# Optimization experiments

Hardware: AMD Instinct MI355X
Metric: run time of the kernel (lower is better)

The kernel has to match this reference:

```python
import jax, jax.numpy as jnp
import numpy as np

DIM = 50
K = 51  # kernel_size == DIM + 1 (required by the original view())
E = 6   # num_elems
NT = 29 # num_targets
B = 8
DN = ('NCDHW', 'OIDHW', 'NCDHW')


def setup_inputs() -> dict:
    key = jax.random.key(0)
    ks = jax.random.split(key, 14)
    f = jnp.float32
    inp = {
        'x': jax.random.uniform(ks[0], (B, E, DIM, DIM, DIM), dtype=f),
        'sigma': 3.0 * jnp.ones((E,), dtype=f),
        'w1': jax.random.normal(ks[1], (32, E, 3, 3, 3), dtype=f) * 0.1,
        'b1': jnp.full((32,), 0.01, dtype=f),
        'w2': jax.random.normal(ks[2], (64, 32, 3, 3, 3), dtype=f) * 0.05,
        'b2': jnp.full((64,), 0.01, dtype=f),
        'w3': jax.random.normal(ks[3], (128, 64, 3, 3, 3), dtype=f) * 0.05,
        'b3': jnp.full((128,), 0.01, dtype=f),
        'w4': jax.random.normal(ks[4], (256, 128, 3, 3, 3), dtype=f) * 0.03,
        'b4': jnp.full((256,), 0.01, dtype=f),
        'fw1': jax.random.normal(ks[5], (128, 256), dtype=f) * 0.06,
        'fb1': jnp.full((128,), 0.01, dtype=f),
        'fw2': jax.random.normal(ks[6], (NT, 128), dtype=f) * 0.08,
        'fb2': jnp.full((NT,), 0.01, dtype=f),
    }
    return inp


def _blur_kernel(sigma):
    # Gauss transformation kernel, shape (E, 1, K, K, K)
    c = jnp.arange(K, dtype=jnp.float32)
    mean = (K - 1) / 2.0
    d2 = (c - mean) ** 2
    # squared radius grid (K,K,K), symmetric so the torch transpose(3,0) axis swap is a no-op
    r2 = d2[:, None, None] + d2[None, :, None] + d2[None, None, :]
    var = sigma ** 2  # (E,)
    a = 1.0 / (2.0 * np.pi * var)  # (E,)
    kern = a[:, None, None, None] * jnp.exp(-r2[None] / (2.0 * var)[:, None, None, None])
    kern = kern / jnp.sum(kern)  # normalize by GLOBAL sum (as in torch code)
    return kern[:, None]  # (E,1,K,K,K)


def _conv3(x, w, b):
    y = jax.lax.conv_general_dilated(x, w, (1, 1, 1), 'VALID', dimension_numbers=DN)
    return y + b[None, :, None, None, None]


def _pool(x):
    return jax.lax.reduce_window(x, -jnp.inf, jax.lax.max,
                                 (1, 1, 2, 2, 2), (1, 1, 2, 2, 2), 'VALID')


def reference(x, sigma, w1, b1, w2, b2, w3, b3, w4, b4, fw1, fb1, fw2, fb2):
    # blur: grouped 3D conv with on-the-fly Gaussian kernel, padding 25 keeps DIM
    kern = _blur_kernel(sigma)
    pad = (K - 1) // 2
    xc = jax.lax.conv_general_dilated(x, kern, (1, 1, 1), [(pad, pad)] * 3,
                                      feature_group_count=E, dimension_numbers=DN)
    xc = xc / jnp.max(xc)
    # conv stack: (conv -> pool -> relu) x4
    h = jax.nn.relu(_pool(_conv3(xc, w1, b1)))   # (B,32,24,24,24)
    h = jax.nn.relu(_pool(_conv3(h, w2, b2)))    # (B,64,11,11,11)
    h = jax.nn.relu(_pool(_conv3(h, w3, b3)))    # (B,128,4,4,4)
    h = jax.nn.relu(_pool(_conv3(h, w4, b4)))    # (B,256,1,1,1)
    v = h.reshape(x.shape[0], -1)                # (B,256)
    y1 = jax.nn.relu(v @ fw1.T + fb1)
    return y1 @ fw2.T + fb2                      # (B,29)
```

## Files before the change

### kernel.cpp

```cpp
#include <hip/hip_runtime.h>
#include <math.h>

#define DIMX 50
#define KK   51
#define NE   6
#define NB   8
#define NVOX ((size_t)NB * NE * DIMX * DIMX * DIMX)

typedef short bf16x8 __attribute__((ext_vector_type(8)));
typedef float f32x4  __attribute__((ext_vector_type(4)));

__device__ __forceinline__ unsigned short f2bf(float f) {
    unsigned u = __float_as_uint(f);
    u += 0x7fffu + ((u >> 16) & 1u);
    return (unsigned short)(u >> 16);
}
__device__ __forceinline__ float bf2f(unsigned short h) {
    return __uint_as_float((unsigned)h << 16);
}
__device__ __forceinline__ uint4 pack8(const unsigned short v[8]) {
    uint4 q;
    q.x = v[0] | ((unsigned)v[1] << 16);
    q.y = v[2] | ((unsigned)v[3] << 16);
    q.z = v[4] | ((unsigned)v[5] << 16);
    q.w = v[6] | ((unsigned)v[7] << 16);
    return q;
}
__device__ __forceinline__ int offA(int o, int k) {
    return ((((o >> 4) * 2 + (k >> 5)) * 64 + ((k >> 3) & 3) * 16 + (o & 15)) << 3) + (k & 7);
}

__global__ void taps_kernel(const float* __restrict__ sigma,
                            unsigned short* __restrict__ MA, unsigned short* __restrict__ MB,
                            float* __restrict__ maxval) {
    __shared__ float sg[NE * KK];
    __shared__ float sgs[NE * KK];
    __shared__ float ssum[NE];
    int t = threadIdx.x;
    if (t == 0) *maxval = 0.f;
    if (t < NE * KK) {
        int e = t / KK, i = t % KK;
        float d = (float)i - 25.0f;
        float var = sigma[e] * sigma[e];
        sg[t] = expf(-d * d / (2.f * var));
    }
    __syncthreads();
    if (t < NE) {
        float s = 0.f;
        for (int i = 0; i < KK; ++i) s += sg[t * KK + i];
        ssum[t] = s;
    }
    __syncthreads();
    if (t < NE * KK) {
        int e = t / KK;
        float S = 0.f;
        for (int e2 = 0; e2 < NE; ++e2) {
            float var2 = sigma[e2] * sigma[e2];
            float a2 = 1.f / (2.f * (float)M_PI * var2);
            float se = ssum[e2];
            S += a2 * se * se * se;
        }
        float var = sigma[e] * sigma[e];
        float a = 1.f / (2.f * (float)M_PI * var);
        sgs[t] = sg[t] * (a / S);
    }
    __syncthreads();
    const int TOT = 2 * 6 * 4 * 2 * 64 * 8;
    for (int i = t; i < 2 * TOT; i += 512) {
        int which = i / TOT;
        int r = i % TOT;
        int q = r;
        int j = q & 7; q >>= 3;
        int l = q & 63; q >>= 6;
        int kc = q & 1; q >>= 1;
        int tile = q & 3; q >>= 2;
        int e = q % 6; q /= 6;
        int hl = q;
        int own = tile * 16 + (l & 15);
        int k   = kc * 32 + ((l >> 4) << 3) + j;
        float v = 0.f;
        if (own < 50 && k < 50) {
            int d = k - own + 25;
            if (d >= 0 && d < KK) v = (which == 0 ? sg : sgs)[e * KK + d];
        }
        unsigned short h = f2bf(v);
        unsigned short out = (hl == 0) ? h : f2bf(v - bf2f(h));
        (which == 0 ? MA : MB)[r] = out;
    }
}

__global__ __launch_bounds__(64)
void blur_k1(const float* __restrict__ in, float* __restrict__ W1,
             const unsigned short* __restrict__ MA) {
    const int l = threadIdx.x, lm = l & 15, lg = l >> 4;
    const int y = blockIdx.x % 50, be = blockIdx.x / 50, e = be % 6;
    const float* pb = in + (size_t)be * 125000 + y * 50;
    bf16x8 Ah[4][2], Al[4][2];
#pragma unroll
    for (int ozt = 0; ozt < 4; ++ozt)
#pragma unroll
        for (int kc = 0; kc < 2; ++kc) {
            Ah[ozt][kc] = *(const bf16x8*)(MA + (((size_t)(0 * 6 + e) * 4 + ozt) * 2 + kc) * 512 + l * 8);
            Al[ozt][kc] = *(const bf16x8*)(MA + (((size_t)(1 * 6 + e) * 4 + ozt) * 2 + kc) * 512 + l * 8);
        }
    float* ob = W1 + (size_t)be * 125000 + y * 50;
    const f32x4 z4 = {0.f, 0.f, 0.f, 0.f};
#pragma unroll 1
    for (int xt = 0; xt < 4; ++xt) {
        const int xx = xt * 16 + lm;
        bf16x8 bh[2], bl[2];
#pragma unroll
        for (int kc = 0; kc < 2; ++kc) {
            unsigned short vh[8], vl[8];
#pragma unroll
            for (int j = 0; j < 8; ++j) {
                int z = kc * 32 + lg * 8 + j;
                float v = (z < 50 && xx < 50) ? pb[(size_t)z * 2500 + xx] : 0.f;
                unsigned short h = f2bf(v);
                vh[j] = h; vl[j] = f2bf(v - bf2f(h));
            }
            uint4 qh = pack8(vh), ql = pack8(vl);
            bh[kc] = *(bf16x8*)&qh; bl[kc] = *(bf16x8*)&ql;
        }
        f32x4 acc[4];
#pragma unroll
        for (int ozt = 0; ozt < 4; ++ozt) acc[ozt] = z4;
#pragma unroll
        for (int ozt = 0; ozt < 4; ++ozt)
#pragma unroll
            for (int kc = 0; kc < 2; ++kc) {
                acc[ozt] = __builtin_amdgcn_mfma_f32_16x16x32_bf16(Ah[ozt][kc], bh[kc], acc[ozt], 0, 0, 0);
                acc[ozt] = __builtin_amdgcn_mfma_f32_16x16x32_bf16(Ah[ozt][kc], bl[kc], acc[ozt], 0, 0, 0);
                acc[ozt] = __builtin_amdgcn_mfma_f32_16x16x32_bf16(Al[ozt][kc], bh[kc], acc[ozt], 0, 0, 0);
            }
        if (xx < 50) {
#pragma unroll
            for (int ozt = 0; ozt < 4; ++ozt)
#pragma unroll
                for (int i = 0; i < 4; ++i) {
                    int oz = ozt * 16 + lg * 4 + i;
                    if (oz < 50) ob[(size_t)oz * 2500 + xx] = acc[ozt][i];
                }
        }
    }
}

__global__ __launch_bounds__(64)
void blur_k2(const float* __restrict__ W1, const unsigned short* __restrict__ MA,
             const unsigned short* __restrict__ MB, unsigned short* __restrict__ X1,
             float* __restrict__ maxval) {
    __shared__ unsigned short Qhi[4096], Qlo[4096];
    const int l = threadIdx.x, lm = l & 15, lg = l >> 4;
    const int q8 = (int)(gridDim.x >> 3);
    const int logical = ((int)blockIdx.x & 7) * q8 + ((int)blockIdx.x >> 3);
    const int e = logical % 6, bz = logical / 6, z = bz % 50, b = bz / 50;
    const float* pb = W1 + (size_t)(b * 6 + e) * 125000 + (size_t)z * 2500;
    bf16x8 Bh[4][2], Bl[4][2];
#pragma unroll
    for (int xt = 0; xt < 4; ++xt) {
        const int xx = xt * 16 + lm;
#pragma unroll
        for (int kc = 0; kc < 2; ++kc) {
            unsigned short vh[8], vl[8];
#pragma unroll
            for (int j = 0; j < 8; ++j) {
                int yy = kc * 32 + lg * 8 + j;
                float v = (yy < 50 && xx < 50) ? pb[yy * 50 + xx] : 0.f;
                unsigned short h = f2bf(v);
                vh[j] = h; vl[j] = f2bf(v - bf2f(h));
            }
            uint4 qh = pack8(vh), ql = pack8(vl);
            Bh[xt][kc] = *(bf16x8*)&qh; Bl[xt][kc] = *(bf16x8*)&ql;
        }
    }
    const f32x4 z4 = {0.f, 0.f, 0.f, 0.f};
#pragma unroll 1
    for (int oyt = 0; oyt < 4; ++oyt) {
        bf16x8 Ah[2], Al[2];
#pragma unroll
        for (int kc = 0; kc < 2; ++kc) {
            Ah[kc] = *(const bf16x8*)(MA + (((size_t)(0 * 6 + e) * 4 + oyt) * 2 + kc) * 512 + l * 8);
            Al[kc] = *(const bf16x8*)(MA + (((size_t)(1 * 6 + e) * 4 + oyt) * 2 + kc) * 512 + l * 8);
        }
#pragma unroll
        for (int xt = 0; xt < 4; ++xt) {
            f32x4 acc = z4;
#pragma unroll
            for (int kc = 0; kc < 2; ++kc) {
                acc = __builtin_amdgcn_mfma_f32_16x16x32_bf16(Ah[kc], Bh[xt][kc], acc, 0, 0, 0);
                acc = __builtin_amdgcn_mfma_f32_16x16x32_bf16(Ah[kc], Bl[xt][kc], acc, 0, 0, 0);
                acc = __builtin_amdgcn_mfma_f32_16x16x32_bf16(Al[kc], Bh[xt][kc], acc, 0, 0, 0);
            }
#pragma unroll
            for (int i = 0; i < 4; ++i) {
                int oy = oyt * 16 + lg * 4 + i;
                int xx = xt * 16 + lm;
                float qv = acc[i];
                unsigned short h = f2bf(qv);
                int off = offA(oy, xx);
                Qhi[off] = h; Qlo[off] = f2bf(qv - bf2f(h));
            }
        }
    }
    __builtin_amdgcn_wave_barrier();
    asm volatile("s_waitcnt lgkmcnt(0)" ::: "memory");
    __builtin_amdgcn_sched_barrier(0);
    float mmax = 0.f;
    unsigned short* xb = X1 + ((size_t)b * 125000 + (size_t)z * 2500) * 8 + e;
#pragma unroll 1
    for (int oyt = 0; oyt < 4; ++oyt) {
        bf16x8 Qh[2], Ql[2];
#pragma unroll
        for (int kc = 0; kc < 2; ++kc) {
            Qh[kc] = *(const bf16x8*)(Qhi + ((oyt * 2 + kc) * 64 + l) * 8);
            Ql[kc] = *(const bf16x8*)(Qlo + ((oyt * 2 + kc) * 64 + l) * 8);
        }
#pragma unroll
        for (int oxt = 0; oxt < 4; ++oxt) {
            f32x4 acc = z4;
#pragma unroll
            for (int kc = 0; kc < 2; ++kc) {
                bf16x8 mh = *(const bf16x8*)(MB + (((size_t)(0 * 6 + e) * 4 + oxt) * 2 + kc) * 512 + l * 8);
                bf16x8 ml = *(const bf16x8*)(MB + (((size_t)(1 * 6 + e) * 4 + oxt) * 2 + kc) * 512 + l * 8);
                acc = __builtin_amdgcn_mfma_f32_16x16x32_bf16(Qh[kc], mh, acc, 0, 0, 0);
                acc = __builtin_amdgcn_mfma_f32_16x16x32_bf16(Qh[kc], ml, acc, 0, 0, 0);
                acc = __builtin_amdgcn_mfma_f32_16x16x32_bf16(Ql[kc], mh, acc, 0, 0, 0);
            }
            int ox = oxt * 16 + lm;
            if (ox < 50) {
#pragma unroll
                for (int i = 0; i < 4; ++i) {
                    int oy = oyt * 16 + lg * 4 + i;
                    if (oy < 50) {
                        float r = acc[i];
                        xb[((size_t)oy * 50 + ox) * 8] = f2bf(r);
                        mmax = fmaxf(mmax, r);
                    }
                }
            }
        }
    }
    for (int o = 32; o; o >>= 1) mmax = fmaxf(mmax, __shfl_xor(mmax, o));
    if (l == 0) atomicMax((int*)maxval, __float_as_int(mmax));
}

__global__ void wprep_kernel(const float* __restrict__ W, unsigned short* __restrict__ out,
                             int CIN, int NCH, int NCOG) {
    int idx = blockIdx.x * 256 + threadIdx.x;
    int total = NCOG * 27 * NCH * 64;
    if (idx >= total) return;
    int l = idx & 63;
    int r = idx >> 6;
    int ch = r % NCH; r /= NCH;
    int tap = r % 27;
    int cog = r / 27;
    int co = cog * 16 + (l & 15);
    unsigned short v[8];
#pragma unroll
    for (int j = 0; j < 8; ++j) {
        int ci = ch * 32 + (l >> 4) * 8 + j;
        v[j] = (ci < CIN) ? f2bf(W[((size_t)co * CIN + ci) * 27 + tap]) : (unsigned short)0;
    }
    ((uint4*)out)[idx] = pack8(v);
}

__global__ void wprep1_kernel(const float* __restrict__ W, unsigned short* __restrict__ out) {
    int idx = blockIdx.x * 64 + threadIdx.x;
    if (idx >= 2 * 9 * 64) return;
    int l = idx & 63;
    int r = idx >> 6;
    int tg = r % 9;
    int cog = r / 9;
    int xsel = l >> 4;
    int co = cog * 16 + (l & 15);
    unsigned short v[8];
#pragma unroll
    for (int j = 0; j < 8; ++j) {
        float wv = 0.f;
        if (j < 6 && xsel < 3) wv = W[((size_t)co * 6 + j) * 27 + tg * 3 + xsel];
        v[j] = f2bf(wv);
    }
    ((uint4*)out)[idx] = pack8(v);
}

__global__ __launch_bounds__(64, 3)
void conv1_mfma(const unsigned short* __restrict__ X8, const unsigned short* __restrict__ wp1,
                const float* __restrict__ bias, const float* __restrict__ maxval,
                unsigned short* __restrict__ X2) {
    const int l = threadIdx.x, lm = l & 15, lg = l >> 4;
    const int q = (int)(gridDim.x >> 3);
    const int bid = ((int)blockIdx.x & 7) * q + ((int)blockIdx.x >> 3);
    const int s0 = bid * 8;
    const int r0 = s0 / 72;
    const int cog = r0 % 2;
    const int pz  = (r0 / 2) % 24;
    const int b   = r0 / 48;
    uint4 B9[9];
    const uint4* wpb = (const uint4*)wp1 + cog * 9 * 64;
#pragma unroll
    for (int t = 0; t < 9; ++t) B9[t] = wpb[t * 64 + l];
    const float rmv = 1.0f / (*maxval);
    const float bia = bias[cog * 16 + lm];
    const unsigned short* Xb = X8 + (size_t)b * 125000 * 8;
    const f32x4 z4 = {0.f, 0.f, 0.f, 0.f};
#pragma unroll 1
    for (int si = 0; si < 8; ++si) {
        const int sid = s0 + si;
        const int xs = sid % 3;
        const int py = (sid / 3) % 24;
        const int x0 = xs * 16;
        f32x4 acc[2][2];
#pragma unroll
        for (int cz = 0; cz < 2; ++cz)
#pragma unroll
            for (int cy = 0; cy < 2; ++cy) acc[cz][cy] = z4;
#pragma unroll
        for (int zi = 0; zi < 4; ++zi) {
            const int zin = 2 * pz + zi;
#pragma unroll
            for (int yi = 0; yi < 4; ++yi) {
                const int yin = 2 * py + yi;
                const unsigned short* rowb = Xb + (size_t)(zin * 50 + yin) * 50 * 8;
                bf16x8 a = *(const bf16x8*)(rowb + (x0 + lm + lg) * 8);
#pragma unroll
                for (int cz = 0; cz < 2; ++cz) {
                    const int kz = zi - cz;
                    if (kz < 0 || kz > 2) continue;
#pragma unroll
                    for (int cy = 0; cy < 2; ++cy) {
                        const int ky = yi - cy;
                        if (ky < 0 || ky > 2) continue;
                        acc[cz][cy] = __builtin_amdgcn_mfma_f32_16x16x32_bf16(
                            a, *(const bf16x8*)&B9[kz * 3 + ky], acc[cz][cy], 0, 0, 0);
                    }
                }
            }
        }
        const int co = cog * 16 + lm;
#pragma unroll
        for (int ip = 0; ip < 2; ++ip) {
            float m0 = fmaxf(fmaxf(acc[0][0][2 * ip], acc[0][1][2 * ip]),
                             fmaxf(acc[1][0][2 * ip], acc[1][1][2 * ip]));
            float m1 = fmaxf(fmaxf(acc[0][0][2 * ip + 1], acc[0][1][2 * ip + 1]),
                             fmaxf(acc[1][0][2 * ip + 1], acc[1][1][2 * ip + 1]));
            float o = fmaxf(fmaxf(m0, m1) * rmv + bia, 0.f);
            int px = x0 / 2 + lg * 2 + ip;
            X2[((((size_t)b * 24 + pz) * 24 + py) * 24 + px) * 32 + co] = f2bf(o);
        }
    }
}

template <int DIN, int DP, int CI, int NCH, int NCOG, int NPY, int NXS, int SPB, int NPZ>
__global__ __launch_bounds__(64, 3)
void convN_mfma(const unsigned short* __restrict__ X, const unsigned short* __restrict__ wp,
                const float* __restrict__ bias, unsigned short* __restrict__ Y, int COUT) {
    const int l = threadIdx.x, lm = l & 15, lg = l >> 4;
    const int qq = (int)(gridDim.x >> 3);
    const int bid = ((int)blockIdx.x & 7) * qq + ((int)blockIdx.x >> 3);
    const int s0 = bid * SPB;
    const int r0 = s0 / (NPY * NXS);
    const int cog = r0 % NCOG;
    const int pz  = (r0 / NCOG) % NPZ;
    const int b   = r0 / (NCOG * NPZ);
    const float bia = bias[cog * 16 + lm];
    const unsigned short* Xb = X + (size_t)b * DIN * DIN * DIN * CI;
    const uint4* wp4 = (const uint4*)wp;
    const f32x4 z4 = {0.f, 0.f, 0.f, 0.f};
#pragma unroll 1
    for (int si = 0; si < SPB; ++si) {
        const int sid = s0 + si;
        const int xs = sid % NXS;
        const int py = (sid / NXS) % NPY;
        const int x0 = xs * 16;
        int xo[3];
#pragma unroll
        for (int kx = 0; kx < 3; ++kx) {
            int xin = x0 + kx + lm;
            if (xin > DIN - 1) xin = DIN - 1;
            xo[kx] = xin * CI + lg * 8;
        }
        f32x4 acc[2][2];
#pragma unroll
        for (int cz = 0; cz < 2; ++cz)
#pragma unroll
            for (int cy = 0; cy < 2; ++cy) acc[cz][cy] = z4;
#pragma unroll 1
        for (int ch = 0; ch < NCH; ++ch) {
            uint4 B[27];
            const uint4* wpb = wp4 + ((size_t)cog * 27 * NCH + ch) * 64;
#pragma unroll
            for (int t = 0; t < 27; ++t) B[t] = wpb[(size_t)t * NCH * 64 + l];
            const unsigned short* Xc = Xb + ch * 32;
#pragma unroll
            for (int zi = 0; zi < 4; ++zi) {
                const int zin = 2 * pz + zi;
#pragma unroll
                for (int yi = 0; yi < 4; ++yi) {
                    const int yin = 2 * py + yi;
                    const unsigned short* rowb = Xc + (size_t)(zin * DIN + yin) * DIN * CI;
#pragma unroll
                    for (int kx = 0; kx < 3; ++kx) {
                        bf16x8 a = *(const bf16x8*)(rowb + xo[kx]);
#pragma unroll
                        for (int cz = 0; cz < 2; ++cz) {
                            const int kz = zi - cz;
                            if (kz < 0 || kz > 2) continue;
#pragma unroll
                            for (int cy = 0; cy < 2; ++cy) {
                                const int ky = yi - cy;
                                if (ky < 0 || ky > 2) continue;
                                const int tap = (kz * 3 + ky) * 3 + kx;
                                acc[cz][cy] = __builtin_amdgcn_mfma_f32_16x16x32_bf16(
                                    a, *(const bf16x8*)&B[tap], acc[cz][cy], 0, 0, 0);
                            }
                        }
                    }
                }
            }
        }
        const int co = cog * 16 + lm;
#pragma unroll
        for (int ip = 0; ip < 2; ++ip) {
            float m0 = fmaxf(fmaxf(acc[0][0][2 * ip], acc[0][1][2 * ip]),
                             fmaxf(acc[1][0][2 * ip], acc[1][1][2 * ip]));
            float m1 = fmaxf(fmaxf(acc[0][0][2 * ip + 1], acc[0][1][2 * ip + 1]),
                             fmaxf(acc[1][0][2 * ip + 1], acc[1][1][2 * ip + 1]));
            float o = fmaxf(fmaxf(m0, m1) + bia, 0.f);
            int px = x0 / 2 + lg * 2 + ip;
            if (px < DP)
                Y[((((size_t)b * DP + pz) * DP + py) * DP + px) * COUT + co] = f2bf(o);
        }
    }
}

__global__ void conv4_kernel(const unsigned short* __restrict__ X4, const float* __restrict__ w,
                             const float* __restrict__ bias, float* __restrict__ out) {
    int wid = (int)((blockIdx.x * blockDim.x + threadIdx.x) >> 6);
    int lane = threadIdx.x & 63;
    if (wid >= NB * 256) return;
    int b = wid >> 8, co = wid & 255;
    float acc[8];
#pragma unroll
    for (int i = 0; i < 8; ++i) acc[i] = 0.f;
    for (int half = 0; half < 2; ++half) {
        int ci = lane + half * 64;
        float win[64];
#pragma unroll
        for (int v = 0; v < 64; ++v)
            win[v] = bf2f(X4[((size_t)b * 64 + v) * 128 + ci]);
        const float* wc = w + ((size_t)co * 128 + ci) * 27;
        float wr[27];
#pragma unroll
        for (int i = 0; i < 27; ++i) wr[i] = wc[i];
#pragma unroll
        for (int kz = 0; kz < 3; ++kz)
#pragma unroll
            for (int ky = 0; ky < 3; ++ky)
#pragma unroll
                for (int kx = 0; kx < 3; ++kx) {
                    float wv = wr[(kz * 3 + ky) * 3 + kx];
#pragma unroll
                    for (int oz = 0; oz < 2; ++oz)
#pragma unroll
                        for (int oy = 0; oy < 2; ++oy)
#pragma unroll
                            for (int ox = 0; ox < 2; ++ox)
                                acc[(oz * 2 + oy) * 2 + ox] =
                                    fmaf(wv, win[((oz + kz) * 4 + (oy + ky)) * 4 + ox + kx],
                                         acc[(oz * 2 + oy) * 2 + ox]);
                }
    }
#pragma unroll
    for (int o = 32; o; o >>= 1)
#pragma unroll
        for (int i = 0; i < 8; ++i) acc[i] += __shfl_xor(acc[i], o);
    if (lane == 0) {
        float m = acc[0];
#pragma unroll
        for (int i = 1; i < 8; ++i) m = fmaxf(m, acc[i]);
        out[(size_t)b * 256 + co] = fmaxf(m + bias[co], 0.f);
    }
}

__global__ void head_kernel(const float* __restrict__ v,
                            const float* __restrict__ fw1, const float* __restrict__ fb1,
                            const float* __restrict__ fw2, const float* __restrict__ fb2,
                            float* __restrict__ out) {
    int b = blockIdx.x, t = threadIdx.x;
    __shared__ float sv[256];
    __shared__ float s1[128];
    sv[t] = v[b * 256 + t];
    sv[t + 128] = v[b * 256 + t + 128];
    __syncthreads();
    float acc = fb1[t];
    const float* wr = fw1 + t * 256;
    for (int k = 0; k < 256; ++k) acc = fmaf(wr[k], sv[k], acc);
    s1[t] = fmaxf(acc, 0.f);
    __syncthreads();
    if (t < 29) {
        float a2 = fb2[t];
        const float* w2 = fw2 + t * 128;
        for (int k = 0; k < 128; ++k) a2 = fmaf(w2[k], s1[k], a2);
        out[b * 29 + t] = a2;
    }
}

extern "C" void kernel_launch(void* const* d_in, const int* in_sizes, int n_in,
                              void* d_out, int out_size, void* d_ws, size_t ws_size,
                              hipStream_t stream) {
    const float* x     = (const float*)d_in[0];
    const float* sigma = (const float*)d_in[1];
    const float* w1    = (const float*)d_in[2];
    const float* b1    = (const float*)d_in[3];
    const float* w2    = (const float*)d_in[4];
    const float* b2    = (const float*)d_in[5];
    const float* w3    = (const float*)d_in[6];
    const float* b3    = (const float*)d_in[7];
    const float* w4    = (const float*)d_in[8];
    const float* b4    = (const float*)d_in[9];
    const float* fw1   = (const float*)d_in[10];
    const float* fb1   = (const float*)d_in[11];
    const float* fw2   = (const float*)d_in[12];
    const float* fb2   = (const float*)d_in[13];
    float* out = (float*)d_out;

    float* W1 = (float*)d_ws;
    unsigned short* X1  = (unsigned short*)(W1 + NVOX);
    unsigned short* X2  = X1 + 8000064;
    unsigned short* X3  = X2 + 3538944;
    unsigned short* X4  = X3 + 681472;
    unsigned short* wp1 = X4 + 65536;
    unsigned short* wp2 = wp1 + 9216;
    unsigned short* wp3 = wp2 + 55296;
    unsigned short* MA  = wp3 + 221184;
    unsigned short* MB  = MA + 49152;
    float* mx = (float*)(MB + 49152);
    float* v4 = mx + 1;

    taps_kernel<<<1, 512, 0, stream>>>(sigma, MA, MB, mx);

    blur_k1<<<NB * NE * 50, 64, 0, stream>>>(x, W1, MA);
    blur_k2<<<NB * NE * 50, 64, 0, stream>>>(W1, MA, MB, X1, mx);

    wprep1_kernel<<<18, 64, 0, stream>>>(w1, wp1);
    wprep_kernel<<<27, 256, 0, stream>>>(w2, wp2, 32, 1, 4);
    wprep_kernel<<<108, 256, 0, stream>>>(w3, wp3, 64, 2, 8);

    conv1_mfma<<<3456, 64, 0, stream>>>(X1, wp1, b1, mx, X2);
    convN_mfma<24, 11, 32, 1, 4, 11, 2, 2, 11><<<3872, 64, 0, stream>>>(X2, wp2, b2, X3, 64);
    convN_mfma<11, 4, 64, 2, 8, 4, 1, 1, 4><<<1024, 64, 0, stream>>>(X3, wp3, b3, X4, 128);

    conv4_kernel<<<512, 256, 0, stream>>>(X4, w4, b4, v4);
    head_kernel<<<8, 128, 0, stream>>>(v4, fw1, fb1, fw2, fb2, out);
}
```

Measured before the change: 205.5 us.

## Split blur tile loops across four waves and merge weight-prep launches

```diff
diff --git a/kernel.cpp b/kernel.cpp
--- a/kernel.cpp
+++ b/kernel.cpp
@@ -89,10 +89,12 @@
     }
 }
 
-__global__ __launch_bounds__(64)
+__global__ __launch_bounds__(256)
 void blur_k1(const float* __restrict__ in, float* __restrict__ W1,
              const unsigned short* __restrict__ MA) {
-    const int l = threadIdx.x, lm = l & 15, lg = l >> 4;
+    const int t = threadIdx.x;
+    const int l = t & 63, lm = l & 15, lg = (l >> 4);
+    const int xt = __builtin_amdgcn_readfirstlane(t >> 6);
     const int y = blockIdx.x % 50, be = blockIdx.x / 50, e = be % 6;
     const float* pb = in + (size_t)be * 125000 + y * 50;
     bf16x8 Ah[4][2], Al[4][2];
@@ -105,52 +107,51 @@
         }
     float* ob = W1 + (size_t)be * 125000 + y * 50;
     const f32x4 z4 = {0.f, 0.f, 0.f, 0.f};
-#pragma unroll 1
-    for (int xt = 0; xt < 4; ++xt) {
-        const int xx = xt * 16 + lm;
-        bf16x8 bh[2], bl[2];
+    const int xx = xt * 16 + lm;
+    bf16x8 bh[2], bl[2];
+#pragma unroll
+    for (int kc = 0; kc < 2; ++kc) {
+        unsigned short vh[8], vl[8];
+#pragma unroll
+        for (int j = 0; j < 8; ++j) {
+            int z = kc * 32 + lg * 8 + j;
+            float v = (z < 50 && xx < 50) ? pb[(size_t)z * 2500 + xx] : 0.f;
+            unsigned short h = f2bf(v);
+            vh[j] = h; vl[j] = f2bf(v - bf2f(h));
+        }
+        uint4 qh = pack8(vh), ql = pack8(vl);
+        bh[kc] = *(bf16x8*)&qh; bl[kc] = *(bf16x8*)&ql;
+    }
+    f32x4 acc[4];
+#pragma unroll
+    for (int ozt = 0; ozt < 4; ++ozt) acc[ozt] = z4;
+#pragma unroll
+    for (int ozt = 0; ozt < 4; ++ozt)
 #pragma unroll
         for (int kc = 0; kc < 2; ++kc) {
-            unsigned short vh[8], vl[8];
-#pragma unroll
-            for (int j = 0; j < 8; ++j) {
-                int z = kc * 32 + lg * 8 + j;
-                float v = (z < 50 && xx < 50) ? pb[(size_t)z * 2500 + xx] : 0.f;
-                unsigned short h = f2bf(v);
-                vh[j] = h; vl[j] = f2bf(v - bf2f(h));
-            }
-            uint4 qh = pack8(vh), ql = pack8(vl);
-            bh[kc] = *(bf16x8*)&qh; bl[kc] = *(bf16x8*)&ql;
-        }
-        f32x4 acc[4];
-#pragma unroll
-        for (int ozt = 0; ozt < 4; ++ozt) acc[ozt] = z4;
+            acc[ozt] = __builtin_amdgcn_mfma_f32_16x16x32_bf16(Ah[ozt][kc], bh[kc], acc[ozt], 0, 0, 0);
+            acc[ozt] = __builtin_amdgcn_mfma_f32_16x16x32_bf16(Ah[ozt][kc], bl[kc], acc[ozt], 0, 0, 0);
+            acc[ozt] = __builtin_amdgcn_mfma_f32_16x16x32_bf16(Al[ozt][kc], bh[kc], acc[ozt], 0, 0, 0);
+        }
+    if (xx < 50) {
 #pragma unroll
         for (int ozt = 0; ozt < 4; ++ozt)
 #pragma unroll
-            for (int kc = 0; kc < 2; ++kc) {
-                acc[ozt] = __builtin_amdgcn_mfma_f32_16x16x32_bf16(Ah[ozt][kc], bh[kc], acc[ozt], 0, 0, 0);
-                acc[ozt] = __builtin_amdgcn_mfma_f32_16x16x32_bf16(Ah[ozt][kc], bl[kc], acc[ozt], 0, 0, 0);
-                acc[ozt] = __builtin_amdgcn_mfma_f32_16x16x32_bf16(Al[ozt][kc], bh[kc], acc[ozt], 0, 0, 0);
-            }
-        if (xx < 50) {
-#pragma unroll
-            for (int ozt = 0; ozt < 4; ++ozt)
-#pragma unroll
-                for (int i = 0; i < 4; ++i) {
-                    int oz = ozt * 16 + lg * 4 + i;
-                    if (oz < 50) ob[(size_t)oz * 2500 + xx] = acc[ozt][i];
-                }
-        }
-    }
-}
-
-__global__ __launch_bounds__(64)
+            for (int i = 0; i < 4; ++i) {
+                int oz = ozt * 16 + lg * 4 + i;
+                if (oz < 50) ob[(size_t)oz * 2500 + xx] = acc[ozt][i];
+            }
+    }
+}
+
+__global__ __launch_bounds__(256)
 void blur_k2(const float* __restrict__ W1, const unsigned short* __restrict__ MA,
              const unsigned short* __restrict__ MB, unsigned short* __restrict__ X1,
              float* __restrict__ maxval) {
     __shared__ unsigned short Qhi[4096], Qlo[4096];
-    const int l = threadIdx.x, lm = l & 15, lg = l >> 4;
+    const int t = threadIdx.x;
+    const int l = t & 63, lm = l & 15, lg = (l >> 4);
+    const int oyt = __builtin_amdgcn_readfirstlane(t >> 6);
     const int q8 = (int)(gridDim.x >> 3);
     const int logical = ((int)blockIdx.x & 7) * q8 + ((int)blockIdx.x >> 3);
     const int e = logical % 6, bz = logical / 6, z = bz % 50, b = bz / 50;
@@ -174,8 +175,7 @@
         }
     }
     const f32x4 z4 = {0.f, 0.f, 0.f, 0.f};
-#pragma unroll 1
-    for (int oyt = 0; oyt < 4; ++oyt) {
+    {
         bf16x8 Ah[2], Al[2];
 #pragma unroll
         for (int kc = 0; kc < 2; ++kc) {
@@ -207,35 +207,32 @@
     __builtin_amdgcn_sched_barrier(0);
     float mmax = 0.f;
     unsigned short* xb = X1 + ((size_t)b * 125000 + (size_t)z * 2500) * 8 + e;
-#pragma unroll 1
-    for (int oyt = 0; oyt < 4; ++oyt) {
-        bf16x8 Qh[2], Ql[2];
+    bf16x8 Qh[2], Ql[2];
+#pragma unroll
+    for (int kc = 0; kc < 2; ++kc) {
+        Qh[kc] = *(const bf16x8*)(Qhi + ((oyt * 2 + kc) * 64 + l) * 8);
+        Ql[kc] = *(const bf16x8*)(Qlo + ((oyt * 2 + kc) * 64 + l) * 8);
+    }
+#pragma unroll
+    for (int oxt = 0; oxt < 4; ++oxt) {
+        f32x4 acc = z4;
 #pragma unroll
         for (int kc = 0; kc < 2; ++kc) {
-            Qh[kc] = *(const bf16x8*)(Qhi + ((oyt * 2 + kc) * 64 + l) * 8);
-            Ql[kc] = *(const bf16x8*)(Qlo + ((oyt * 2 + kc) * 64 + l) * 8);
-        }
-#pragma unroll
-        for (int oxt = 0; oxt < 4; ++oxt) {
-            f32x4 acc = z4;
-#pragma unroll
-            for (int kc = 0; kc < 2; ++kc) {
-                bf16x8 mh = *(const bf16x8*)(MB + (((size_t)(0 * 6 + e) * 4 + oxt) * 2 + kc) * 512 + l * 8);
-                bf16x8 ml = *(const bf16x8*)(MB + (((size_t)(1 * 6 + e) * 4 + oxt) * 2 + kc) * 512 + l * 8);
-                acc = __builtin_amdgcn_mfma_f32_16x16x32_bf16(Qh[kc], mh, acc, 0, 0, 0);
-                acc = __builtin_amdgcn_mfma_f32_16x16x32_bf16(Qh[kc], ml, acc, 0, 0, 0);
-                acc = __builtin_amdgcn_mfma_f32_16x16x32_bf16(Ql[kc], mh, acc, 0, 0, 0);
-            }
-            int ox = oxt * 16 + lm;
-            if (ox < 50) {
-#pragma unroll
-                for (int i = 0; i < 4; ++i) {
-                    int oy = oyt * 16 + lg * 4 + i;
-                    if (oy < 50) {
-                        float r = acc[i];
-                        xb[((size_t)oy * 50 + ox) * 8] = f2bf(r);
-                        mmax = fmaxf(mmax, r);
-                    }
+            bf16x8 mh = *(const bf16x8*)(MB + (((size_t)(0 * 6 + e) * 4 + oxt) * 2 + kc) * 512 + l * 8);
+            bf16x8 ml = *(const bf16x8*)(MB + (((size_t)(1 * 6 + e) * 4 + oxt) * 2 + kc) * 512 + l * 8);
+            acc = __builtin_amdgcn_mfma_f32_16x16x32_bf16(Qh[kc], mh, acc, 0, 0, 0);
+            acc = __builtin_amdgcn_mfma_f32_16x16x32_bf16(Qh[kc], ml, acc, 0, 0, 0);
+            acc = __builtin_amdgcn_mfma_f32_16x16x32_bf16(Ql[kc], mh, acc, 0, 0, 0);
+        }
+        int ox = oxt * 16 + lm;
+        if (ox < 50) {
+#pragma unroll
+            for (int i = 0; i < 4; ++i) {
+                int oy = oyt * 16 + lg * 4 + i;
+                if (oy < 50) {
+                    float r = acc[i];
+                    xb[((size_t)oy * 50 + ox) * 8] = f2bf(r);
+                    mmax = fmaxf(mmax, r);
                 }
             }
         }
@@ -244,43 +241,61 @@
     if (l == 0) atomicMax((int*)maxval, __float_as_int(mmax));
 }
 
-__global__ void wprep_kernel(const float* __restrict__ W, unsigned short* __restrict__ out,
-                             int CIN, int NCH, int NCOG) {
+__global__ void wprep_all(const float* __restrict__ W1c, const float* __restrict__ W2c,
+                          const float* __restrict__ W3c,
+                          unsigned short* __restrict__ wp1, unsigned short* __restrict__ wp2,
+                          unsigned short* __restrict__ wp3) {
     int idx = blockIdx.x * 256 + threadIdx.x;
-    int total = NCOG * 27 * NCH * 64;
-    if (idx >= total) return;
-    int l = idx & 63;
-    int r = idx >> 6;
-    int ch = r % NCH; r /= NCH;
-    int tap = r % 27;
-    int cog = r / 27;
-    int co = cog * 16 + (l & 15);
-    unsigned short v[8];
-#pragma unroll
-    for (int j = 0; j < 8; ++j) {
-        int ci = ch * 32 + (l >> 4) * 8 + j;
-        v[j] = (ci < CIN) ? f2bf(W[((size_t)co * CIN + ci) * 27 + tap]) : (unsigned short)0;
-    }
-    ((uint4*)out)[idx] = pack8(v);
-}
-
-__global__ void wprep1_kernel(const float* __restrict__ W, unsigned short* __restrict__ out) {
-    int idx = blockIdx.x * 64 + threadIdx.x;
-    if (idx >= 2 * 9 * 64) return;
-    int l = idx & 63;
-    int r = idx >> 6;
-    int tg = r % 9;
-    int cog = r / 9;
-    int xsel = l >> 4;
-    int co = cog * 16 + (l & 15);
-    unsigned short v[8];
-#pragma unroll
-    for (int j = 0; j < 8; ++j) {
-        float wv = 0.f;
-        if (j < 6 && xsel < 3) wv = W[((size_t)co * 6 + j) * 27 + tg * 3 + xsel];
-        v[j] = f2bf(wv);
-    }
-    ((uint4*)out)[idx] = pack8(v);
+    const int N1 = 2 * 9 * 64;
+    const int N2 = 4 * 27 * 1 * 64;
+    const int N3 = 8 * 27 * 2 * 64;
+    if (idx < N1) {
+        int l = idx & 63;
+        int r = idx >> 6;
+        int tg = r % 9, cog = r / 9;
+        int xsel = l >> 4;
+        int co = cog * 16 + (l & 15);
+        unsigned short v[8];
+#pragma unroll
+        for (int j = 0; j < 8; ++j) {
+            float wv = 0.f;
+            if (j < 6 && xsel < 3) wv = W1c[((size_t)co * 6 + j) * 27 + tg * 3 + xsel];
+            v[j] = f2bf(wv);
+        }
+        ((uint4*)wp1)[idx] = pack8(v);
+        return;
+    }
+    idx -= N1;
+    if (idx < N2) {
+        int l = idx & 63;
+        int r = idx >> 6;
+        int tap = r % 27, cog = r / 27;
+        int co = cog * 16 + (l & 15);
+        unsigned short v[8];
+#pragma unroll
+        for (int j = 0; j < 8; ++j) {
+            int ci = (l >> 4) * 8 + j;
+            v[j] = f2bf(W2c[((size_t)co * 32 + ci) * 27 + tap]);
+        }
+        ((uint4*)wp2)[idx] = pack8(v);
+        return;
+    }
+    idx -= N2;
+    if (idx < N3) {
+        int l = idx & 63;
+        int r = idx >> 6;
+        int ch = r % 2; r /= 2;
+        int tap = r % 27;
+        int cog = r / 27;
+        int co = cog * 16 + (l & 15);
+        unsigned short v[8];
+#pragma unroll
+        for (int j = 0; j < 8; ++j) {
+            int ci = ch * 32 + (l >> 4) * 8 + j;
+            v[j] = f2bf(W3c[((size_t)co * 64 + ci) * 27 + tap]);
+        }
+        ((uint4*)wp3)[idx] = pack8(v);
+    }
 }
 
 __global__ __launch_bounds__(64, 3)
@@ -539,12 +554,10 @@
 
     taps_kernel<<<1, 512, 0, stream>>>(sigma, MA, MB, mx);
 
-    blur_k1<<<NB * NE * 50, 64, 0, stream>>>(x, W1, MA);
-    blur_k2<<<NB * NE * 50, 64, 0, stream>>>(W1, MA, MB, X1, mx);
-
-    wprep1_kernel<<<18, 64, 0, stream>>>(w1, wp1);
-    wprep_kernel<<<27, 256, 0, stream>>>(w2, wp2, 32, 1, 4);
-    wprep_kernel<<<108, 256, 0, stream>>>(w3, wp3, 64, 2, 8);
+    blur_k1<<<NB * NE * 50, 256, 0, stream>>>(x, W1, MA);
+    blur_k2<<<NB * NE * 50, 256, 0, stream>>>(W1, MA, MB, X1, mx);
+
+    wprep_all<<<140, 256, 0, stream>>>(w1, w2, w3, wp1, wp2, wp3);
 
     conv1_mfma<<<3456, 64, 0, stream>>>(X1, wp1, b1, mx, X2);
     convN_mfma<24, 11, 32, 1, 4, 11, 2, 2, 11><<<3872, 64, 0, stream>>>(X2, wp2, b2, X3, 64);
```

Measured after the change: 260.3 us. +26.7%, slower.
